# Kernel tuning notes

Measured on AMD Instinct MI355X. Metric: run time of the kernel, lower is better.

Reference implementation:

```python
import jax, jax.numpy as jnp
import numpy as np


def setup_inputs() -> dict:
    key = jax.random.key(0)
    k1, k2 = jax.random.split(key)
    N = 50000
    E = 800000
    out_features = 64
    edge = jax.random.randint(k1, (2, E), 0, N, dtype=jnp.int64)
    edge_w = jax.random.normal(k2, (E, out_features), dtype=jnp.float32)
    return {"edge": edge, "edge_w": edge_w, "N": N, "E": E, "out_features": out_features}


def reference(edge, edge_w, N, E, out_features):
    # sparse_coo_tensor(edge, edge_w, [N, N, F]) summed over dim=1 reduces to a
    # segment-sum of edge values over the row (source) index edge[0].
    # output[i, f] = sum_{e: edge[0,e]==i} edge_w[e, f]   -> [N, out_features]
    return jax.ops.segment_sum(edge_w, edge[0], num_segments=N)
```

## Files before the change

### kernel.cpp

```cpp
#include <hip/hip_runtime.h>


#define TILE 1024

__global__ __launch_bounds__(256) void hist_rank_kernel(
    const int* __restrict__ edge0, int* __restrict__ counts,
    int* __restrict__ rank, int E)
{
    int t = blockIdx.x * blockDim.x + threadIdx.x;
    int base = t * 4;
    if (base + 3 < E) {
        int4 r = ((const int4*)edge0)[t];
        int4 k;
        k.x = atomicAdd(&counts[r.x], 1);
        k.y = atomicAdd(&counts[r.y], 1);
        k.z = atomicAdd(&counts[r.z], 1);
        k.w = atomicAdd(&counts[r.w], 1);
        ((int4*)rank)[t] = k;
    } else {
        for (int i = base; i < E; ++i) rank[i] = atomicAdd(&counts[edge0[i]], 1);
    }
}

__global__ __launch_bounds__(256) void scan_partial(
    const int* __restrict__ counts, int* __restrict__ tileSum, int N)
{
    __shared__ int wsum[4];
    int t = threadIdx.x;
    int base = blockIdx.x * TILE + t * 4;
    int s = 0;
    #pragma unroll
    for (int k = 0; k < 4; ++k) {
        int i = base + k;
        if (i < N) s += counts[i];
    }
    for (int off = 1; off < 64; off <<= 1) s += __shfl_xor(s, off);
    if ((t & 63) == 0) wsum[t >> 6] = s;
    __syncthreads();
    if (t == 0) tileSum[blockIdx.x] = wsum[0] + wsum[1] + wsum[2] + wsum[3];
}

__global__ __launch_bounds__(256) void scan_final(
    const int* __restrict__ counts, const int* __restrict__ tileSum,
    int* __restrict__ offsets, int N, int E, int numTiles)
{
    __shared__ int wtot[4];
    __shared__ int tilePre;
    int t = threadIdx.x;
    int lane = t & 63, wv = t >> 6;

    if (t < 64) {
        int v0 = (t < numTiles) ? tileSum[t] : 0;
        int v = v0;
        #pragma unroll
        for (int off = 1; off < 64; off <<= 1) {
            int u = __shfl_up(v, off);
            if (t >= off) v += u;
        }
        if (t == blockIdx.x) tilePre = v - v0;
    }
    if (blockIdx.x == 0 && t == 0) offsets[N] = E;

    int base = blockIdx.x * TILE + t * 4;
    int c[4]; int s = 0;
    #pragma unroll
    for (int k = 0; k < 4; ++k) {
        int i = base + k;
        c[k] = (i < N) ? counts[i] : 0;
        s += c[k];
    }
    int inc = s;
    #pragma unroll
    for (int off = 1; off < 64; off <<= 1) {
        int u = __shfl_up(inc, off);
        if (lane >= off) inc += u;
    }
    if (lane == 63) wtot[wv] = inc;
    __syncthreads();
    int wpre = 0;
    for (int w = 0; w < wv; ++w) wpre += wtot[w];
    int pre = tilePre + wpre + (inc - s);
    #pragma unroll
    for (int k = 0; k < 4; ++k) {
        int i = base + k;
        if (i < N) offsets[i] = pre;
        pre += c[k];
    }
}

__global__ __launch_bounds__(256) void scatter_kernel(
    const int* __restrict__ edge0, const int* __restrict__ rank,
    const int* __restrict__ offsets, int* __restrict__ ids, int E)
{
    int t = blockIdx.x * blockDim.x + threadIdx.x;
    int base = t * 4;
    if (base + 3 < E) {
        int4 r = ((const int4*)edge0)[t];
        int4 k = ((const int4*)rank)[t];
        ids[offsets[r.x] + k.x] = base;
        ids[offsets[r.y] + k.y] = base + 1;
        ids[offsets[r.z] + k.z] = base + 2;
        ids[offsets[r.w] + k.w] = base + 3;
    } else {
        for (int i = base; i < E; ++i) ids[offsets[edge0[i]] + rank[i]] = i;
    }
}

__global__ __launch_bounds__(256) void reduce_kernel(
    const int* __restrict__ offsets, const int* __restrict__ ids,
    const float4* __restrict__ w4, float4* __restrict__ out4, int N)
{
    int row = blockIdx.x * 4 + (threadIdx.x >> 6);
    if (row >= N) return;
    int lane = threadIdx.x & 63;
    int sub = lane >> 3, g = lane & 7;
    int beg = offsets[row], end = offsets[row + 1];
    int deg = end - beg;

    float4 a0 = make_float4(0.f, 0.f, 0.f, 0.f);
    float4 a1 = make_float4(0.f, 0.f, 0.f, 0.f);

    int nloc = deg < 64 ? deg : 64;
    int myid = (lane < deg) ? ids[beg + lane] : 0;

    const float4* __restrict__ wp = w4 + g * 2;

    int full = nloc & ~15;
    for (int b = 0; b < full; b += 16) {
        int e0 = __shfl(myid, b + sub);
        int e1 = __shfl(myid, b + 8 + sub);
        float4 w00 = wp[(size_t)e0 * 16];
        float4 w01 = wp[(size_t)e0 * 16 + 1];
        float4 w10 = wp[(size_t)e1 * 16];
        float4 w11 = wp[(size_t)e1 * 16 + 1];
        a0.x += w00.x + w10.x; a0.y += w00.y + w10.y;
        a0.z += w00.z + w10.z; a0.w += w00.w + w10.w;
        a1.x += w01.x + w11.x; a1.y += w01.y + w11.y;
        a1.z += w01.z + w11.z; a1.w += w01.w + w11.w;
    }
    if (full < nloc) {
        int s0 = full + sub;
        int s1 = full + 8 + sub;
        int e0 = __shfl(myid, s0 & 63);
        int e1 = __shfl(myid, s1 & 63);
        if (s0 < nloc) {
            float4 w0 = wp[(size_t)e0 * 16];
            float4 w1 = wp[(size_t)e0 * 16 + 1];
            a0.x += w0.x; a0.y += w0.y; a0.z += w0.z; a0.w += w0.w;
            a1.x += w1.x; a1.y += w1.y; a1.z += w1.z; a1.w += w1.w;
        }
        if (s1 < nloc) {
            float4 w0 = wp[(size_t)e1 * 16];
            float4 w1 = wp[(size_t)e1 * 16 + 1];
            a0.x += w0.x; a0.y += w0.y; a0.z += w0.z; a0.w += w0.w;
            a1.x += w1.x; a1.y += w1.y; a1.z += w1.z; a1.w += w1.w;
        }
    }
    for (int j = beg + 64 + sub; j < end; j += 8) {
        int e = ids[j];
        float4 w0 = wp[(size_t)e * 16];
        float4 w1 = wp[(size_t)e * 16 + 1];
        a0.x += w0.x; a0.y += w0.y; a0.z += w0.z; a0.w += w0.w;
        a1.x += w1.x; a1.y += w1.y; a1.z += w1.z; a1.w += w1.w;
    }

    #pragma unroll
    for (int m = 8; m < 64; m <<= 1) {
        a0.x += __shfl_xor(a0.x, m); a0.y += __shfl_xor(a0.y, m);
        a0.z += __shfl_xor(a0.z, m); a0.w += __shfl_xor(a0.w, m);
        a1.x += __shfl_xor(a1.x, m); a1.y += __shfl_xor(a1.y, m);
        a1.z += __shfl_xor(a1.z, m); a1.w += __shfl_xor(a1.w, m);
    }
    if (sub == 0) {
        out4[(size_t)row * 16 + g * 2]     = a0;
        out4[(size_t)row * 16 + g * 2 + 1] = a1;
    }
}

extern "C" void kernel_launch(void* const* d_in, const int* in_sizes, int n_in,
                              void* d_out, int out_size, void* d_ws, size_t ws_size,
                              hipStream_t stream) {
    const int*   edge   = (const int*)d_in[0];
    const float* edge_w = (const float*)d_in[1];
    int E = in_sizes[0] / 2;
    int N = out_size / 64;
    int numTiles = (N + TILE - 1) / TILE;

    int* counts  = (int*)d_ws;
    int* offsets = counts + N;
    int* rank    = offsets + N + 1;
    int* ids     = rank + E;
    int* tileSum = ids + E;

    (void)hipMemsetAsync(counts, 0, (size_t)N * sizeof(int), stream);

    int blocksE = (E + 1023) / 1024;
    hist_rank_kernel<<<blocksE, 256, 0, stream>>>(edge, counts, rank, E);
    scan_partial<<<numTiles, 256, 0, stream>>>(counts, tileSum, N);
    scan_final<<<numTiles, 256, 0, stream>>>(counts, tileSum, offsets, N, E, numTiles);
    scatter_kernel<<<blocksE, 256, 0, stream>>>(edge, rank, offsets, ids, E);

    int blocksR = (N + 3) / 4;
    reduce_kernel<<<blocksR, 256, 0, stream>>>(offsets, ids, (const float4*)edge_w,
                                               (float4*)d_out, N);
}
```

Before: 351.8 us.

## Replace global-atomic CSR build with two-level bucketed radix sort

Replaces the global atomic histogram/rank, two-pass scan and random scatter with a bucket-based counting sort. Edges are first histogrammed into 256-row buckets per 4096-edge chunk in LDS, a single-block scan produces the bucket offsets, and records are staged in LDS and written coalesced. A per-bucket kernel then builds the row offsets and ids locally in LDS. This targets global atomic contention and uncoalesced scatter writes. The costs are a serial single-block scan over NB*nblk entries and an extra pass through the intermediate records.

Result: no change. 354.5 us (+0.8%).

```diff
diff --git a/kernel.cpp b/kernel.cpp
--- a/kernel.cpp
+++ b/kernel.cpp
@@ -1,109 +1,193 @@
 #include <hip/hip_runtime.h>
 
 
-#define TILE 1024
-
-__global__ __launch_bounds__(256) void hist_rank_kernel(
-    const int* __restrict__ edge0, int* __restrict__ counts,
-    int* __restrict__ rank, int E)
-{
-    int t = blockIdx.x * blockDim.x + threadIdx.x;
-    int base = t * 4;
-    if (base + 3 < E) {
-        int4 r = ((const int4*)edge0)[t];
-        int4 k;
-        k.x = atomicAdd(&counts[r.x], 1);
-        k.y = atomicAdd(&counts[r.y], 1);
-        k.z = atomicAdd(&counts[r.z], 1);
-        k.w = atomicAdd(&counts[r.w], 1);
-        ((int4*)rank)[t] = k;
-    } else {
-        for (int i = base; i < E; ++i) rank[i] = atomicAdd(&counts[edge0[i]], 1);
-    }
-}
-
-__global__ __launch_bounds__(256) void scan_partial(
-    const int* __restrict__ counts, int* __restrict__ tileSum, int N)
-{
-    __shared__ int wsum[4];
-    int t = threadIdx.x;
-    int base = blockIdx.x * TILE + t * 4;
-    int s = 0;
-    #pragma unroll
-    for (int k = 0; k < 4; ++k) {
-        int i = base + k;
-        if (i < N) s += counts[i];
-    }
-    for (int off = 1; off < 64; off <<= 1) s += __shfl_xor(s, off);
-    if ((t & 63) == 0) wsum[t >> 6] = s;
-    __syncthreads();
-    if (t == 0) tileSum[blockIdx.x] = wsum[0] + wsum[1] + wsum[2] + wsum[3];
-}
-
-__global__ __launch_bounds__(256) void scan_final(
-    const int* __restrict__ counts, const int* __restrict__ tileSum,
-    int* __restrict__ offsets, int N, int E, int numTiles)
-{
-    __shared__ int wtot[4];
-    __shared__ int tilePre;
-    int t = threadIdx.x;
-    int lane = t & 63, wv = t >> 6;
-
-    if (t < 64) {
-        int v0 = (t < numTiles) ? tileSum[t] : 0;
-        int v = v0;
+#define CEDGE 4096
+#define WROWS 256
+#define SHIFT 8
+#define STCAP 8192
+
+__global__ __launch_bounds__(256) void bucket_hist(
+    const int* __restrict__ edge0, int* __restrict__ cnt,
+    int E, int nblk, int NB)
+{
+    __shared__ int lh[256];
+    int t = threadIdx.x, blk = blockIdx.x;
+    lh[t] = 0;
+    __syncthreads();
+    #pragma unroll
+    for (int j = 0; j < 4; ++j) {
+        int idx4 = blk * 1024 + j * 256 + t;
+        int base = idx4 * 4;
+        if (base + 3 < E) {
+            int4 r = ((const int4*)edge0)[idx4];
+            atomicAdd(&lh[r.x >> SHIFT], 1);
+            atomicAdd(&lh[r.y >> SHIFT], 1);
+            atomicAdd(&lh[r.z >> SHIFT], 1);
+            atomicAdd(&lh[r.w >> SHIFT], 1);
+        } else {
+            for (int i = base; i < E && i < base + 4; ++i)
+                atomicAdd(&lh[edge0[i] >> SHIFT], 1);
+        }
+    }
+    __syncthreads();
+    if (t < NB) cnt[t * nblk + blk] = lh[t];
+}
+
+__global__ __launch_bounds__(1024) void scan_flat(int* __restrict__ a, int M)
+{
+    __shared__ int wsums[16];
+    __shared__ int carryS;
+    int t = threadIdx.x, lane = t & 63, wv = t >> 6;
+    if (t == 0) carryS = 0;
+    __syncthreads();
+    for (int base = 0; base < M; base += 1024) {
+        int i = base + t;
+        int v = (i < M) ? a[i] : 0;
+        int inc = v;
         #pragma unroll
         for (int off = 1; off < 64; off <<= 1) {
-            int u = __shfl_up(v, off);
-            if (t >= off) v += u;
-        }
-        if (t == blockIdx.x) tilePre = v - v0;
-    }
-    if (blockIdx.x == 0 && t == 0) offsets[N] = E;
-
-    int base = blockIdx.x * TILE + t * 4;
-    int c[4]; int s = 0;
-    #pragma unroll
-    for (int k = 0; k < 4; ++k) {
-        int i = base + k;
-        c[k] = (i < N) ? counts[i] : 0;
-        s += c[k];
-    }
-    int inc = s;
+            int u = __shfl_up(inc, off);
+            if (lane >= off) inc += u;
+        }
+        if (lane == 63) wsums[wv] = inc;
+        __syncthreads();
+        int wpre = 0;
+        for (int w = 0; w < wv; ++w) wpre += wsums[w];
+        int c = carryS;
+        if (i < M) a[i] = c + wpre + inc - v;
+        __syncthreads();
+        if (t == 1023) carryS = c + wpre + inc;
+    }
+}
+
+__global__ __launch_bounds__(256) void bucket_scatter(
+    const int* __restrict__ edge0, const int* __restrict__ cntS,
+    int* __restrict__ recs , int E, int nblk, int NB)
+{
+    __shared__ int lh[256];
+    __shared__ int so[256];
+    __shared__ int gb[256];
+    __shared__ int ws4[4];
+    __shared__ int2 stage[CEDGE];
+    int t = threadIdx.x, lane = t & 63, wv = t >> 6, blk = blockIdx.x;
+    lh[t] = 0;
+    if (t < NB) gb[t] = cntS[t * nblk + blk];
+    __syncthreads();
+
+    int rowR[16], rkR[16];
+    #pragma unroll
+    for (int j = 0; j < 4; ++j) {
+        int idx4 = blk * 1024 + j * 256 + t;
+        int base = idx4 * 4;
+        if (base + 3 < E) {
+            int4 r = ((const int4*)edge0)[idx4];
+            rowR[j*4+0] = r.x; rkR[j*4+0] = atomicAdd(&lh[r.x >> SHIFT], 1);
+            rowR[j*4+1] = r.y; rkR[j*4+1] = atomicAdd(&lh[r.y >> SHIFT], 1);
+            rowR[j*4+2] = r.z; rkR[j*4+2] = atomicAdd(&lh[r.z >> SHIFT], 1);
+            rowR[j*4+3] = r.w; rkR[j*4+3] = atomicAdd(&lh[r.w >> SHIFT], 1);
+        } else {
+            #pragma unroll
+            for (int c = 0; c < 4; ++c) {
+                int i = base + c;
+                if (i < E) {
+                    int rr = edge0[i];
+                    rowR[j*4+c] = rr;
+                    rkR[j*4+c]  = atomicAdd(&lh[rr >> SHIFT], 1);
+                } else {
+                    rowR[j*4+c] = -1;
+                    rkR[j*4+c]  = 0;
+                }
+            }
+        }
+    }
+    __syncthreads();
+    {
+        int v = lh[t];
+        int inc = v;
+        #pragma unroll
+        for (int off = 1; off < 64; off <<= 1) {
+            int u = __shfl_up(inc, off);
+            if (lane >= off) inc += u;
+        }
+        if (lane == 63) ws4[wv] = inc;
+        __syncthreads();
+        int wpre = 0;
+        for (int w = 0; w < wv; ++w) wpre += ws4[w];
+        so[t] = wpre + inc - v;
+    }
+    __syncthreads();
+    #pragma unroll
+    for (int k = 0; k < 16; ++k) {
+        int row = rowR[k];
+        if (row >= 0) {
+            int b = row >> SHIFT;
+            int id = blk * CEDGE + ((k >> 2) * 256 + t) * 4 + (k & 3);
+            stage[so[b] + rkR[k]] = make_int2(row, id);
+        }
+    }
+    __syncthreads();
+    int Ctot = E - blk * CEDGE; if (Ctot > CEDGE) Ctot = CEDGE;
+    int2* rout = (int2*)recs;
+    for (int p = t; p < Ctot; p += 256) {
+        int2 rec = stage[p];
+        int b = rec.x >> SHIFT;
+        rout[gb[b] + (p - so[b])] = rec;
+    }
+}
+
+__global__ __launch_bounds__(1024) void bucket_csr(
+    const int* __restrict__ cntS, const int* __restrict__ recs,
+    int* __restrict__ offsets, int* __restrict__ ids,
+    int E, int nblk, int NB, int N)
+{
+    __shared__ int rowCnt[WROWS];
+    __shared__ int rowFill[WROWS];
+    __shared__ int rowPre[WROWS];
+    __shared__ int ws4[4];
+    __shared__ int stage[STCAP];
+    int t = threadIdx.x, b = blockIdx.x;
+    int lane = t & 63, wv = t >> 6;
+    int S0 = cntS[b * nblk];
+    int S1 = (b + 1 < NB) ? cntS[(b + 1) * nblk] : E;
+    int cnt = S1 - S0;
+    if (t < WROWS) { rowCnt[t] = 0; rowFill[t] = 0; }
+    __syncthreads();
+    const int2* rin = (const int2*)recs;
+    for (int k = t; k < cnt; k += 1024) {
+        int2 r = rin[S0 + k];
+        atomicAdd(&rowCnt[r.x - (b << SHIFT)], 1);
+    }
+    __syncthreads();
+    int v = (t < WROWS) ? rowCnt[t] : 0;
+    int inc = v;
     #pragma unroll
     for (int off = 1; off < 64; off <<= 1) {
         int u = __shfl_up(inc, off);
         if (lane >= off) inc += u;
     }
-    if (lane == 63) wtot[wv] = inc;
-    __syncthreads();
-    int wpre = 0;
-    for (int w = 0; w < wv; ++w) wpre += wtot[w];
-    int pre = tilePre + wpre + (inc - s);
-    #pragma unroll
-    for (int k = 0; k < 4; ++k) {
-        int i = base + k;
-        if (i < N) offsets[i] = pre;
-        pre += c[k];
-    }
-}
-
-__global__ __launch_bounds__(256) void scatter_kernel(
-    const int* __restrict__ edge0, const int* __restrict__ rank,
-    const int* __restrict__ offsets, int* __restrict__ ids, int E)
-{
-    int t = blockIdx.x * blockDim.x + threadIdx.x;
-    int base = t * 4;
-    if (base + 3 < E) {
-        int4 r = ((const int4*)edge0)[t];
-        int4 k = ((const int4*)rank)[t];
-        ids[offsets[r.x] + k.x] = base;
-        ids[offsets[r.y] + k.y] = base + 1;
-        ids[offsets[r.z] + k.z] = base + 2;
-        ids[offsets[r.w] + k.w] = base + 3;
-    } else {
-        for (int i = base; i < E; ++i) ids[offsets[edge0[i]] + rank[i]] = i;
-    }
+    if (lane == 63 && wv < 4) ws4[wv] = inc;
+    __syncthreads();
+    if (t < WROWS) {
+        int wpre = 0;
+        for (int w = 0; w < wv; ++w) wpre += ws4[w];
+        int ex = wpre + inc - v;
+        rowPre[t] = ex;
+        int gr = (b << SHIFT) + t;
+        if (gr < N) offsets[gr] = S0 + ex;
+    }
+    if (b == NB - 1 && t == 0) offsets[N] = E;
+    __syncthreads();
+    bool inLds = (cnt <= STCAP);
+    for (int k = t; k < cnt; k += 1024) {
+        int2 r = rin[S0 + k];
+        int lr = r.x - (b << SHIFT);
+        int pos = rowPre[lr] + atomicAdd(&rowFill[lr], 1);
+        if (inLds) stage[pos] = r.y;
+        else       ids[S0 + pos] = r.y;
+    }
+    __syncthreads();
+    if (inLds)
+        for (int k = t; k < cnt; k += 1024) ids[S0 + k] = stage[k];
 }
 
 __global__ __launch_bounds__(256) void reduce_kernel(
@@ -184,23 +268,20 @@
     const float* edge_w = (const float*)d_in[1];
     int E = in_sizes[0] / 2;
     int N = out_size / 64;
-    int numTiles = (N + TILE - 1) / TILE;
-
-    int* counts  = (int*)d_ws;
-    int* offsets = counts + N;
-    int* rank    = offsets + N + 1;
-    int* ids     = rank + E;
-    int* tileSum = ids + E;
-
-    (void)hipMemsetAsync(counts, 0, (size_t)N * sizeof(int), stream);
-
-    int blocksE = (E + 1023) / 1024;
-    hist_rank_kernel<<<blocksE, 256, 0, stream>>>(edge, counts, rank, E);
-    scan_partial<<<numTiles, 256, 0, stream>>>(counts, tileSum, N);
-    scan_final<<<numTiles, 256, 0, stream>>>(counts, tileSum, offsets, N, E, numTiles);
-    scatter_kernel<<<blocksE, 256, 0, stream>>>(edge, rank, offsets, ids, E);
+    int nblk = (E + CEDGE - 1) / CEDGE;
+    int NB   = (N + WROWS - 1) / WROWS;
+
+    int* recs    = (int*)d_ws;
+    int* cntS    = recs + 2 * (size_t)E;
+    int* offsets = cntS + (size_t)NB * nblk;
+    int* ids     = offsets + N + 1;
+
+    bucket_hist   <<<nblk, 256, 0, stream>>>(edge, cntS, E, nblk, NB);
+    scan_flat     <<<1, 1024, 0, stream>>>(cntS, NB * nblk);
+    bucket_scatter<<<nblk, 256, 0, stream>>>(edge, cntS, recs, E, nblk, NB);
+    bucket_csr    <<<NB, 1024, 0, stream>>>(cntS, recs, offsets, ids, E, nblk, NB, N);
 
     int blocksR = (N + 3) / 4;
-    reduce_kernel<<<blocksR, 256, 0, stream>>>(offsets, ids, (const float4*)edge_w,
-                                               (float4*)d_out, N);
-}
+    reduce_kernel <<<blocksR, 256, 0, stream>>>(offsets, ids, (const float4*)edge_w,
+                                                (float4*)d_out, N);
+}
```

## Replace CSR sort-and-reduce pipeline with single fused float atomic scatter kernel

Applied to the files above, without the earlier changes.

Drops the histogram, two-pass scan, scatter and per-row gather-reduce kernels. A single kernel now streams edge weights contiguously and atomically adds each float into the zeroed output row given by edge0. This removes four kernel launches and the index build traffic, but issues 51.2M float atomics to L2. It also makes summation order nondeterministic.

Measured after the change: 893.1 us. +153.8%, slower.

```diff
diff --git a/kernel.cpp b/kernel.cpp
--- a/kernel.cpp
+++ b/kernel.cpp
@@ -1,179 +1,43 @@
 #include <hip/hip_runtime.h>
 
 
-#define TILE 1024
+#define UN 4
 
-__global__ __launch_bounds__(256) void hist_rank_kernel(
-    const int* __restrict__ edge0, int* __restrict__ counts,
-    int* __restrict__ rank, int E)
+__global__ __launch_bounds__(256) void fused_atomic_spmm(
+    const int* __restrict__ edge0, const float4* __restrict__ w4,
+    float* __restrict__ out, int E)
 {
-    int t = blockIdx.x * blockDim.x + threadIdx.x;
-    int base = t * 4;
-    if (base + 3 < E) {
-        int4 r = ((const int4*)edge0)[t];
-        int4 k;
-        k.x = atomicAdd(&counts[r.x], 1);
-        k.y = atomicAdd(&counts[r.y], 1);
-        k.z = atomicAdd(&counts[r.z], 1);
-        k.w = atomicAdd(&counts[r.w], 1);
-        ((int4*)rank)[t] = k;
+    int g = blockIdx.x * blockDim.x + threadIdx.x;
+    int f = g & 15;
+    int e0 = (g >> 4) * UN;
+    if (e0 >= E) return;
+
+    if (e0 + UN <= E) {
+        int4 er = *reinterpret_cast<const int4*>(&edge0[e0]);
+        float4 v0 = w4[(size_t)(e0 + 0) * 16 + f];
+        float4 v1 = w4[(size_t)(e0 + 1) * 16 + f];
+        float4 v2 = w4[(size_t)(e0 + 2) * 16 + f];
+        float4 v3 = w4[(size_t)(e0 + 3) * 16 + f];
+        float* p0 = &out[(size_t)er.x * 64 + f * 4];
+        float* p1 = &out[(size_t)er.y * 64 + f * 4];
+        float* p2 = &out[(size_t)er.z * 64 + f * 4];
+        float* p3 = &out[(size_t)er.w * 64 + f * 4];
+        atomicAdd(p0 + 0, v0.x); atomicAdd(p0 + 1, v0.y);
+        atomicAdd(p0 + 2, v0.z); atomicAdd(p0 + 3, v0.w);
+        atomicAdd(p1 + 0, v1.x); atomicAdd(p1 + 1, v1.y);
+        atomicAdd(p1 + 2, v1.z); atomicAdd(p1 + 3, v1.w);
+        atomicAdd(p2 + 0, v2.x); atomicAdd(p2 + 1, v2.y);
+        atomicAdd(p2 + 2, v2.z); atomicAdd(p2 + 3, v2.w);
+        atomicAdd(p3 + 0, v3.x); atomicAdd(p3 + 1, v3.y);
+        atomicAdd(p3 + 2, v3.z); atomicAdd(p3 + 3, v3.w);
     } else {
-        for (int i = base; i < E; ++i) rank[i] = atomicAdd(&counts[edge0[i]], 1);
-    }
-}
-
-__global__ __launch_bounds__(256) void scan_partial(
-    const int* __restrict__ counts, int* __restrict__ tileSum, int N)
-{
-    __shared__ int wsum[4];
-    int t = threadIdx.x;
-    int base = blockIdx.x * TILE + t * 4;
-    int s = 0;
-    #pragma unroll
-    for (int k = 0; k < 4; ++k) {
-        int i = base + k;
-        if (i < N) s += counts[i];
-    }
-    for (int off = 1; off < 64; off <<= 1) s += __shfl_xor(s, off);
-    if ((t & 63) == 0) wsum[t >> 6] = s;
-    __syncthreads();
-    if (t == 0) tileSum[blockIdx.x] = wsum[0] + wsum[1] + wsum[2] + wsum[3];
-}
-
-__global__ __launch_bounds__(256) void scan_final(
-    const int* __restrict__ counts, const int* __restrict__ tileSum,
-    int* __restrict__ offsets, int N, int E, int numTiles)
-{
-    __shared__ int wtot[4];
-    __shared__ int tilePre;
-    int t = threadIdx.x;
-    int lane = t & 63, wv = t >> 6;
-
-    if (t < 64) {
-        int v0 = (t < numTiles) ? tileSum[t] : 0;
-        int v = v0;
-        #pragma unroll
-        for (int off = 1; off < 64; off <<= 1) {
-            int u = __shfl_up(v, off);
-            if (t >= off) v += u;
+        for (int e = e0; e < E; ++e) {
+            int row = edge0[e];
+            float4 v = w4[(size_t)e * 16 + f];
+            float* p = &out[(size_t)row * 64 + f * 4];
+            atomicAdd(p + 0, v.x); atomicAdd(p + 1, v.y);
+            atomicAdd(p + 2, v.z); atomicAdd(p + 3, v.w);
         }
-        if (t == blockIdx.x) tilePre = v - v0;
-    }
-    if (blockIdx.x == 0 && t == 0) offsets[N] = E;
-
-    int base = blockIdx.x * TILE + t * 4;
-    int c[4]; int s = 0;
-    #pragma unroll
-    for (int k = 0; k < 4; ++k) {
-        int i = base + k;
-        c[k] = (i < N) ? counts[i] : 0;
-        s += c[k];
-    }
-    int inc = s;
-    #pragma unroll
-    for (int off = 1; off < 64; off <<= 1) {
-        int u = __shfl_up(inc, off);
-        if (lane >= off) inc += u;
-    }
-    if (lane == 63) wtot[wv] = inc;
-    __syncthreads();
-    int wpre = 0;
-    for (int w = 0; w < wv; ++w) wpre += wtot[w];
-    int pre = tilePre + wpre + (inc - s);
-    #pragma unroll
-    for (int k = 0; k < 4; ++k) {
-        int i = base + k;
-        if (i < N) offsets[i] = pre;
-        pre += c[k];
-    }
-}
-
-__global__ __launch_bounds__(256) void scatter_kernel(
-    const int* __restrict__ edge0, const int* __restrict__ rank,
-    const int* __restrict__ offsets, int* __restrict__ ids, int E)
-{
-    int t = blockIdx.x * blockDim.x + threadIdx.x;
-    int base = t * 4;
-    if (base + 3 < E) {
-        int4 r = ((const int4*)edge0)[t];
-        int4 k = ((const int4*)rank)[t];
-        ids[offsets[r.x] + k.x] = base;
-        ids[offsets[r.y] + k.y] = base + 1;
-        ids[offsets[r.z] + k.z] = base + 2;
-        ids[offsets[r.w] + k.w] = base + 3;
-    } else {
-        for (int i = base; i < E; ++i) ids[offsets[edge0[i]] + rank[i]] = i;
-    }
-}
-
-__global__ __launch_bounds__(256) void reduce_kernel(
-    const int* __restrict__ offsets, const int* __restrict__ ids,
-    const float4* __restrict__ w4, float4* __restrict__ out4, int N)
-{
-    int row = blockIdx.x * 4 + (threadIdx.x >> 6);
-    if (row >= N) return;
-    int lane = threadIdx.x & 63;
-    int sub = lane >> 3, g = lane & 7;
-    int beg = offsets[row], end = offsets[row + 1];
-    int deg = end - beg;
-
-    float4 a0 = make_float4(0.f, 0.f, 0.f, 0.f);
-    float4 a1 = make_float4(0.f, 0.f, 0.f, 0.f);
-
-    int nloc = deg < 64 ? deg : 64;
-    int myid = (lane < deg) ? ids[beg + lane] : 0;
-
-    const float4* __restrict__ wp = w4 + g * 2;
-
-    int full = nloc & ~15;
-    for (int b = 0; b < full; b += 16) {
-        int e0 = __shfl(myid, b + sub);
-        int e1 = __shfl(myid, b + 8 + sub);
-        float4 w00 = wp[(size_t)e0 * 16];
-        float4 w01 = wp[(size_t)e0 * 16 + 1];
-        float4 w10 = wp[(size_t)e1 * 16];
-        float4 w11 = wp[(size_t)e1 * 16 + 1];
-        a0.x += w00.x + w10.x; a0.y += w00.y + w10.y;
-        a0.z += w00.z + w10.z; a0.w += w00.w + w10.w;
-        a1.x += w01.x + w11.x; a1.y += w01.y + w11.y;
-        a1.z += w01.z + w11.z; a1.w += w01.w + w11.w;
-    }
-    if (full < nloc) {
-        int s0 = full + sub;
-        int s1 = full + 8 + sub;
-        int e0 = __shfl(myid, s0 & 63);
-        int e1 = __shfl(myid, s1 & 63);
-        if (s0 < nloc) {
-            float4 w0 = wp[(size_t)e0 * 16];
-            float4 w1 = wp[(size_t)e0 * 16 + 1];
-            a0.x += w0.x; a0.y += w0.y; a0.z += w0.z; a0.w += w0.w;
-            a1.x += w1.x; a1.y += w1.y; a1.z += w1.z; a1.w += w1.w;
-        }
-        if (s1 < nloc) {
-            float4 w0 = wp[(size_t)e1 * 16];
-            float4 w1 = wp[(size_t)e1 * 16 + 1];
-            a0.x += w0.x; a0.y += w0.y; a0.z += w0.z; a0.w += w0.w;
-            a1.x += w1.x; a1.y += w1.y; a1.z += w1.z; a1.w += w1.w;
-        }
-    }
-    for (int j = beg + 64 + sub; j < end; j += 8) {
-        int e = ids[j];
-        float4 w0 = wp[(size_t)e * 16];
-        float4 w1 = wp[(size_t)e * 16 + 1];
-        a0.x += w0.x; a0.y += w0.y; a0.z += w0.z; a0.w += w0.w;
-        a1.x += w1.x; a1.y += w1.y; a1.z += w1.z; a1.w += w1.w;
-    }
-
-    #pragma unroll
-    for (int m = 8; m < 64; m <<= 1) {
-        a0.x += __shfl_xor(a0.x, m); a0.y += __shfl_xor(a0.y, m);
-        a0.z += __shfl_xor(a0.z, m); a0.w += __shfl_xor(a0.w, m);
-        a1.x += __shfl_xor(a1.x, m); a1.y += __shfl_xor(a1.y, m);
-        a1.z += __shfl_xor(a1.z, m); a1.w += __shfl_xor(a1.w, m);
-    }
-    if (sub == 0) {
-        out4[(size_t)row * 16 + g * 2]     = a0;
-        out4[(size_t)row * 16 + g * 2 + 1] = a1;
     }
 }
 
@@ -183,24 +47,11 @@
     const int*   edge   = (const int*)d_in[0];
     const float* edge_w = (const float*)d_in[1];
     int E = in_sizes[0] / 2;
-    int N = out_size / 64;
-    int numTiles = (N + TILE - 1) / TILE;
+    (void)hipMemsetAsync(d_out, 0, (size_t)out_size * sizeof(float), stream);
 
-    int* counts  = (int*)d_ws;
-    int* offsets = counts + N;
-    int* rank    = offsets + N + 1;
-    int* ids     = rank + E;
-    int* tileSum = ids + E;
-
-    (void)hipMemsetAsync(counts, 0, (size_t)N * sizeof(int), stream);
-
-    int blocksE = (E + 1023) / 1024;
-    hist_rank_kernel<<<blocksE, 256, 0, stream>>>(edge, counts, rank, E);
-    scan_partial<<<numTiles, 256, 0, stream>>>(counts, tileSum, N);
-    scan_final<<<numTiles, 256, 0, stream>>>(counts, tileSum, offsets, N, E, numTiles);
-    scatter_kernel<<<blocksE, 256, 0, stream>>>(edge, rank, offsets, ids, E);
-
-    int blocksR = (N + 3) / 4;
-    reduce_kernel<<<blocksR, 256, 0, stream>>>(offsets, ids, (const float4*)edge_w,
-                                               (float4*)d_out, N);
+    int groups  = (E + UN - 1) / UN;
+    long long threads = (long long)groups * 16;
+    int blocks  = (int)((threads + 255) / 256);
+    fused_atomic_spmm<<<blocks, 256, 0, stream>>>(edge, (const float4*)edge_w,
+                                                  (float*)d_out, E);
 }
```
